# Optimization experiments

Measured on AMD Instinct MI355X. Metric: run time of the kernel, lower is better.

The kernel has to match this reference:

```python
import jax, jax.numpy as jnp
import numpy as np

B, L, D, A = 4, 4096, 256, 64  # batch, seq_len, n_embd, att_size

def setup_inputs() -> dict:
    key = jax.random.key(0)
    kx, kq, kk, kv = jax.random.split(key, 4)
    x = jax.random.normal(kx, (B, L, D), dtype=jnp.float32)
    # torch nn.Linear(n_embd, att_size) weight is [att_size, n_embd]; we store transposed [D, A]
    s = 1.0 / np.sqrt(D)
    Wq = jax.random.normal(kq, (D, A), dtype=jnp.float32) * s
    Wk = jax.random.normal(kk, (D, A), dtype=jnp.float32) * s
    Wv = jax.random.normal(kv, (D, A), dtype=jnp.float32) * s
    return {"x": x, "Wq": Wq, "Wk": Wk, "Wv": Wv}

def reference(x, Wq, Wk, Wv):
    # q,k,v: [B,L,A]
    q = jnp.einsum('bld,da->bla', x, Wq)
    k = jnp.einsum('bld,da->bla', x, Wk)
    v = jnp.einsum('bld,da->bla', x, Wv)
    # NOTE: original module does NOT scale by 1/sqrt(att_size)
    scores = jnp.einsum('bqa,bka->bqk', q, k)  # [B,L,L]
    Lq = x.shape[1]
    causal = jnp.tril(jnp.ones((Lq, Lq), dtype=bool))
    scores = jnp.where(causal, scores, -jnp.inf)
    weights = jax.nn.softmax(scores, axis=-1)
    # dropout is identity in eval mode
    out = jnp.einsum('bqk,bka->bqa', weights, v)  # [B,L,A]
    return out
```

## Files before the change

kernel.cpp:

```cpp
#include <hip/hip_runtime.h>
#include <math.h>

#define B_ 4
#define L_ 4096
#define D_ 256
#define A_ 64
#define M_ (B_*L_)

typedef _Float16 half4 __attribute__((ext_vector_type(4)));
typedef _Float16 half8 __attribute__((ext_vector_type(8)));
typedef __attribute__((ext_vector_type(4))) float floatx4;

__device__ __forceinline__ unsigned short f2h_(float f) {
    _Float16 h = (_Float16)f;
    return __builtin_bit_cast(unsigned short, h);
}

__global__ __launch_bounds__(256) void wconv_kernel(
    const float* __restrict__ Wq, const float* __restrict__ Wk,
    const float* __restrict__ Wv, unsigned short* __restrict__ wt)
{
    const int w = blockIdx.x, t = threadIdx.x;
    const float* W = (w == 0) ? Wq : (w == 1) ? Wk : Wv;
    unsigned short* o = wt + w * A_ * D_;
    const float scale = (w == 0) ? 1.44269504f : 1.0f;
    __shared__ float T[A_ * 260];
    #pragma unroll
    for (int p = 0; p < 16; ++p) {
        int idx = p * 256 + t;
        int d = idx >> 4, a4 = (idx & 15) * 4;
        float4 v = *(const float4*)(W + d * A_ + a4);
        T[(a4 + 0) * 260 + d] = v.x * scale;
        T[(a4 + 1) * 260 + d] = v.y * scale;
        T[(a4 + 2) * 260 + d] = v.z * scale;
        T[(a4 + 3) * 260 + d] = v.w * scale;
    }
    __syncthreads();
    const int a = t >> 2, d0 = (t & 3) * 64;
    #pragma unroll
    for (int i = 0; i < 16; ++i) {
        float4 v = *(const float4*)(&T[a * 260 + d0 + 4 * i]);
        ushort4 s;
        s.x = f2h_(v.x); s.y = f2h_(v.y); s.z = f2h_(v.z); s.w = f2h_(v.w);
        *(ushort4*)(o + a * D_ + d0 + 4 * i) = s;
    }
}

__global__ __launch_bounds__(384) void proj_kernel(
    const float* __restrict__ x,
    const unsigned short* __restrict__ wt,
    unsigned short* __restrict__ qo,
    unsigned short* __restrict__ ko,
    unsigned short* __restrict__ vto)
{
    __shared__ __align__(16) unsigned short Xh[32 * 264];
    __shared__ __align__(16) unsigned short Cst[6 * 1536];
    const int t = threadIdx.x, m0 = blockIdx.x * 32;

    #pragma unroll
    for (int p = 0; p < 6; ++p) {
        int idx = p * 384 + t;
        if (idx < 2048) {
            int row = idx >> 6, col = (idx & 63) * 4;
            float4 v = *(const float4*)(x + (size_t)(m0 + row) * D_ + col);
            ushort4 s;
            s.x = f2h_(v.x); s.y = f2h_(v.y); s.z = f2h_(v.z); s.w = f2h_(v.w);
            *(ushort4*)(Xh + row * 264 + col) = s;
        }
    }
    __syncthreads();

    const int wid = t >> 6, lane = t & 63, c = lane & 15, g = lane >> 4;
    const int w = wid >> 1, mt = wid & 1;

    half8 xa[8];
    #pragma unroll
    for (int s = 0; s < 8; ++s)
        xa[s] = *(const half8*)(Xh + (16 * mt + c) * 264 + 32 * s + 8 * g);

    const unsigned short* wsrc = wt + w * A_ * D_;
    unsigned short* Cw = Cst + wid * 1536;
    #pragma unroll
    for (int nt = 0; nt < 4; ++nt) {
        floatx4 acc = {0.f, 0.f, 0.f, 0.f};
        #pragma unroll
        for (int s = 0; s < 8; ++s) {
            half8 wb = *(const half8*)(wsrc + (16 * nt + c) * D_ + 32 * s + 8 * g);
            acc = __builtin_amdgcn_mfma_f32_16x16x32_f16(xa[s], wb, acc, 0, 0, 0);
        }
        if (w < 2) {
            #pragma unroll
            for (int r = 0; r < 4; ++r)
                Cw[(4 * g + r) * 72 + 16 * nt + c] = f2h_(acc[r]);
        } else {
            #pragma unroll
            for (int r = 0; r < 4; ++r)
                Cw[(16 * nt + c) * 24 + 4 * g + r] = f2h_(acc[r]);
        }
    }

    if (w < 2) {
        unsigned short* o = (w == 0) ? qo : ko;
        const int row16 = lane >> 2, seg = lane & 3;
        uint4 d0 = *(const uint4*)(Cw + row16 * 72 + seg * 16);
        uint4 d1 = *(const uint4*)(Cw + row16 * 72 + seg * 16 + 8);
        unsigned short* p = o + (size_t)(m0 + 16 * mt + row16) * A_ + seg * 16;
        *(uint4*)(p) = d0;
        *(uint4*)(p + 8) = d1;
    }
    __syncthreads();
    if (t < 256) {
        const int a = t >> 2, quarter = t & 3;
        const int o = quarter * 8, mtv = o >> 4, idx = o & 15;
        uint4 d = *(const uint4*)(Cst + (4 + mtv) * 1536 + a * 24 + idx);
        const int bb = m0 >> 12, l0 = m0 & (L_ - 1);
        *(uint4*)(vto + ((size_t)(bb * A_ + a)) * L_ + l0 + o) = d;
    }
}

__global__ __launch_bounds__(512) void attn_kernel(
    const unsigned short* __restrict__ qb,
    const unsigned short* __restrict__ kb,
    const unsigned short* __restrict__ vt,
    float* __restrict__ out,
    float* __restrict__ po1,
    float2* __restrict__ ml0,
    float2* __restrict__ ml1)
{
    __shared__ __align__(16) unsigned short smem[4 * 4608];
    unsigned short* Ks = smem;
    unsigned short* Vs = smem + 2 * 4608;

    const int t    = threadIdx.x;
    const int lane = t & 63;
    const int wid  = t >> 6;
    const int qsub = wid >> 1;
    const int ph   = wid & 1;
    const int c    = lane & 15;
    const int g    = lane >> 4;

    const int bx   = blockIdx.x;
    const int slot = bx & 255, rr = bx >> 8;
    const int qt0  = slot >> 2;
    const int h    = slot & 1;
    const int b    = ((slot >> 1) & 1) + 2 * rr;
    const int qt   = rr ? (63 - qt0) : qt0;

    const int q0    = qt * 64;
    const int qrow0 = q0 + 16 * qsub;
    const int qme   = qrow0 + c;

    const size_t base  = (size_t)b * L_ * A_;
    const size_t vbase = (size_t)b * A_ * L_;

    half8 qf[2];
    {
        const unsigned short* qp = qb + base + (size_t)(qrow0 + c) * A_ + g * 8;
        qf[0] = *(const half8*)(qp);
        qf[1] = *(const half8*)(qp + 32);
    }

    floatx4 O4[4];
    #pragma unroll
    for (int at = 0; at < 4; ++at) O4[at] = (floatx4){0.f, 0.f, 0.f, 0.f};
    float m_ = -INFINITY, l_ = 0.f;

    const int T   = qt + 1;
    const int Th  = (T + 1) >> 1;
    const int t0  = h ? Th : 0;
    const int t1  = h ? T : Th;
    const int nIt = (t1 - t0 + 1) >> 1;
    const int Tm1 = T - 1;

    for (int it = 0; it < nIt; ++it) {
        __syncthreads();
        #pragma unroll
        for (int tile = 0; tile < 2; ++tile) {
            const int kts = t0 + 2 * it + tile;
            if (kts < t1) {
                const int k0s = kts << 6;
                const int row = t >> 3, c8 = t & 7;
                uint4 dK = *(const uint4*)(kb + base + (size_t)k0s * 64 + t * 8);
                *(uint4*)(Ks + tile * 4608 + row * 72 + c8 * 8) = dK;
                uint4 dV = *(const uint4*)(vt + vbase + (size_t)row * L_ + k0s + c8 * 8);
                *(uint4*)(Vs + tile * 4608 + row * 72 + c8 * 8) = dV;
            }
        }
        __syncthreads();

        const int kt = t0 + 2 * it + ph;
        if (kt >= t1) continue;
        const int k0 = kt << 6;
        const unsigned short* Kw = Ks + ph * 4608;
        const unsigned short* Vw = Vs + ph * 4608;

        floatx4 S4[4];
        #pragma unroll
        for (int nt = 0; nt < 4; ++nt) S4[nt] = (floatx4){0.f, 0.f, 0.f, 0.f};
        #pragma unroll
        for (int s = 0; s < 2; ++s)
            #pragma unroll
            for (int nt = 0; nt < 4; ++nt) {
                half8 kf = *(const half8*)(Kw + (16 * nt + c) * 72 + 32 * s + 8 * g);
                S4[nt] = __builtin_amdgcn_mfma_f32_16x16x32_f16(kf, qf[s], S4[nt], 0, 0, 0);
            }

        if (kt == Tm1) {
            #pragma unroll
            for (int nt = 0; nt < 4; ++nt)
                #pragma unroll
                for (int r = 0; r < 4; ++r)
                    if (k0 + 16 * nt + 4 * g + r > qme) S4[nt][r] = -INFINITY;
        }

        float tm = fmaxf(fmaxf(fmaxf(S4[0][0], S4[0][1]), fmaxf(S4[0][2], S4[0][3])),
                         fmaxf(fmaxf(S4[1][0], S4[1][1]), fmaxf(S4[1][2], S4[1][3])));
        tm = fmaxf(tm, fmaxf(fmaxf(fmaxf(S4[2][0], S4[2][1]), fmaxf(S4[2][2], S4[2][3])),
                             fmaxf(fmaxf(S4[3][0], S4[3][1]), fmaxf(S4[3][2], S4[3][3]))));
        tm = fmaxf(tm, __shfl_xor(tm, 16));
        tm = fmaxf(tm, __shfl_xor(tm, 32));
        const float mn  = fmaxf(m_, tm);
        const float mnc = fmaxf(mn, -3.0e38f);
        const float al  = exp2f(fminf(m_ - mnc, 0.f));
        float rs = 0.f;
        half4 pf[4];
        #pragma unroll
        for (int nt = 0; nt < 4; ++nt) {
            #pragma unroll
            for (int r = 0; r < 4; ++r) {
                float p = exp2f(S4[nt][r] - mnc);
                S4[nt][r] = p;
                rs += p;
            }
            pf[nt][0] = (_Float16)S4[nt][0];
            pf[nt][1] = (_Float16)S4[nt][1];
            pf[nt][2] = (_Float16)S4[nt][2];
            pf[nt][3] = (_Float16)S4[nt][3];
        }
        rs += __shfl_xor(rs, 16);
        rs += __shfl_xor(rs, 32);
        l_ = l_ * al + rs;
        m_ = mn;

        #pragma unroll
        for (int at = 0; at < 4; ++at) {
            O4[at] *= al;
            #pragma unroll
            for (int nt = 0; nt < 4; ++nt) {
                half4 va = *(const half4*)(Vw + (16 * at + c) * 72 + 16 * nt + 4 * g);
                O4[at] = __builtin_amdgcn_mfma_f32_16x16x16f16(va, pf[nt], O4[at], 0, 0, 0);
            }
        }
    }

    __syncthreads();
    float*  Of  = (float*)smem;
    float2* mlb = (float2*)(smem + 16384);
    #pragma unroll
    for (int at = 0; at < 4; ++at) {
        float4 v; v.x = O4[at][0]; v.y = O4[at][1]; v.z = O4[at][2]; v.w = O4[at][3];
        ((float4*)Of)[wid * 256 + at * 64 + lane] = v;
    }
    if (g == 0) { float2 ml; ml.x = m_; ml.y = l_; mlb[wid * 16 + c] = ml; }
    __syncthreads();

    {
        const int q64 = t >> 3, seg = t & 7;
        const int qs = q64 >> 4, cc = q64 & 15;
        const float2 A0 = mlb[(2 * qs) * 16 + cc];
        const float2 A1 = mlb[(2 * qs + 1) * 16 + cc];
        const float mf = fmaxf(A0.x, A1.x);
        const float mc = fmaxf(mf, -3.0e38f);
        const float w0 = exp2f(A0.x - mc);
        const float w1 = exp2f(A1.x - mc);
        const float ls = w0 * A0.y + w1 * A1.y;
        float res[8];
        #pragma unroll
        for (int u = 0; u < 8; ++u) {
            const int a = seg * 8 + u;
            const int at = a >> 4, gg = (a >> 2) & 3, r = a & 3;
            const int i0 = ((2 * qs) * 256 + at * 64 + gg * 16 + cc) * 4 + r;
            const int i1 = ((2 * qs + 1) * 256 + at * 64 + gg * 16 + cc) * 4 + r;
            res[u] = w0 * Of[i0] + w1 * Of[i1];
        }
        float* PO = h ? po1 : out;
        float* p = PO + (base + (size_t)(q0 + q64) * A_) + seg * 8;
        *(float4*)(p)     = make_float4(res[0], res[1], res[2], res[3]);
        *(float4*)(p + 4) = make_float4(res[4], res[5], res[6], res[7]);
        if (seg == 0) {
            float2 ml; ml.x = mf; ml.y = ls;
            (h ? ml1 : ml0)[b * L_ + q0 + q64] = ml;
        }
    }
}

__global__ __launch_bounds__(256) void merge_kernel(
    float* __restrict__ out, const float* __restrict__ po1,
    const float2* __restrict__ ml0, const float2* __restrict__ ml1)
{
    const int tg = blockIdx.x * 256 + threadIdx.x;
    const int q = tg >> 4;
    const float2 a0 = ml0[q], a1 = ml1[q];
    const float mf = fmaxf(a0.x, a1.x);
    const float mc = fmaxf(mf, -3.0e38f);
    const float w0 = exp2f(a0.x - mc);
    const float w1 = exp2f(a1.x - mc);
    const float inv = 1.f / (w0 * a0.y + w1 * a1.y);
    float4 o0 = ((const float4*)out)[tg];
    float4 o1 = ((const float4*)po1)[tg];
    float4 r;
    r.x = (o0.x * w0 + o1.x * w1) * inv;
    r.y = (o0.y * w0 + o1.y * w1) * inv;
    r.z = (o0.z * w0 + o1.z * w1) * inv;
    r.w = (o0.w * w0 + o1.w * w1) * inv;
    ((float4*)out)[tg] = r;
}

extern "C" void kernel_launch(void* const* d_in, const int* in_sizes, int n_in,
                              void* d_out, int out_size, void* d_ws, size_t ws_size,
                              hipStream_t stream) {
    const float* x  = (const float*)d_in[0];
    const float* Wq = (const float*)d_in[1];
    const float* Wk = (const float*)d_in[2];
    const float* Wv = (const float*)d_in[3];

    char* ws = (char*)d_ws;
    unsigned short* qb = (unsigned short*)(ws);
    unsigned short* kb = (unsigned short*)(ws + (2u << 20));
    unsigned short* vt = (unsigned short*)(ws + (4u << 20));
    unsigned short* wt = (unsigned short*)(ws + (6u << 20));
    float*  po1 = (float*) (ws + (6u << 20) + 98304);
    float2* ml0 = (float2*)(ws + (6u << 20) + 98304 + (4u << 20));
    float2* ml1 = (float2*)(ws + (6u << 20) + 98304 + (4u << 20) + 131072);
    float* out = (float*)d_out;

    hipLaunchKernelGGL(wconv_kernel, dim3(3), dim3(256), 0, stream, Wq, Wk, Wv, wt);
    hipLaunchKernelGGL(proj_kernel, dim3(M_ / 32), dim3(384), 0, stream, x, wt, qb, kb, vt);
    hipLaunchKernelGGL(attn_kernel, dim3(512), dim3(512), 0, stream,
                       qb, kb, vt, out, po1, ml0, ml1);
    hipLaunchKernelGGL(merge_kernel, dim3(1024), dim3(256), 0, stream, out, po1, ml0, ml1);
}
```

Measured before the change: 124.8 us.

## Split attention KV range four ways instead of two and merge four partials

Each query tile's causal KV range is now split into four chunks, handled by 1024 blocks instead of 512, with the block-to-(batch, tile, split) mapping reworked. The merge kernel combines four partial outputs and their max/sum stats. The aim is more parallelism and better load balance across CUs for the triangular workload. The cost is extra partial-output traffic, more workspace, and a heavier merge. Tiles with few KV blocks get empty or tiny splits.

```diff
diff --git a/kernel.cpp b/kernel.cpp
--- a/kernel.cpp
+++ b/kernel.cpp
@@ -124,8 +124,12 @@
     const unsigned short* __restrict__ vt,
     float* __restrict__ out,
     float* __restrict__ po1,
+    float* __restrict__ po2,
+    float* __restrict__ po3,
     float2* __restrict__ ml0,
-    float2* __restrict__ ml1)
+    float2* __restrict__ ml1,
+    float2* __restrict__ ml2,
+    float2* __restrict__ ml3)
 {
     __shared__ __align__(16) unsigned short smem[4 * 4608];
     unsigned short* Ks = smem;
@@ -142,9 +146,9 @@
     const int bx   = blockIdx.x;
     const int slot = bx & 255, rr = bx >> 8;
     const int qt0  = slot >> 2;
-    const int h    = slot & 1;
-    const int b    = ((slot >> 1) & 1) + 2 * rr;
-    const int qt   = rr ? (63 - qt0) : qt0;
+    const int b    = slot & 3;
+    const int h    = rr;
+    const int qt   = (rr < 2) ? qt0 : (63 - qt0);
 
     const int q0    = qt * 64;
     const int qrow0 = q0 + 16 * qsub;
@@ -166,9 +170,8 @@
     float m_ = -INFINITY, l_ = 0.f;
 
     const int T   = qt + 1;
-    const int Th  = (T + 1) >> 1;
-    const int t0  = h ? Th : 0;
-    const int t1  = h ? T : Th;
+    const int t0  = (h * T) >> 2;
+    const int t1  = ((h + 1) * T) >> 2;
     const int nIt = (t1 - t0 + 1) >> 1;
     const int Tm1 = T - 1;
 
@@ -283,36 +286,43 @@
             const int i1 = ((2 * qs + 1) * 256 + at * 64 + gg * 16 + cc) * 4 + r;
             res[u] = w0 * Of[i0] + w1 * Of[i1];
         }
-        float* PO = h ? po1 : out;
+        float* PO = (h == 0) ? out : (h == 1) ? po1 : (h == 2) ? po2 : po3;
         float* p = PO + (base + (size_t)(q0 + q64) * A_) + seg * 8;
         *(float4*)(p)     = make_float4(res[0], res[1], res[2], res[3]);
         *(float4*)(p + 4) = make_float4(res[4], res[5], res[6], res[7]);
         if (seg == 0) {
             float2 ml; ml.x = mf; ml.y = ls;
-            (h ? ml1 : ml0)[b * L_ + q0 + q64] = ml;
+            float2* MLp = (h == 0) ? ml0 : (h == 1) ? ml1 : (h == 2) ? ml2 : ml3;
+            MLp[b * L_ + q0 + q64] = ml;
         }
     }
 }
 
 __global__ __launch_bounds__(256) void merge_kernel(
     float* __restrict__ out, const float* __restrict__ po1,
-    const float2* __restrict__ ml0, const float2* __restrict__ ml1)
+    const float* __restrict__ po2, const float* __restrict__ po3,
+    const float2* __restrict__ ml0, const float2* __restrict__ ml1,
+    const float2* __restrict__ ml2, const float2* __restrict__ ml3)
 {
     const int tg = blockIdx.x * 256 + threadIdx.x;
     const int q = tg >> 4;
-    const float2 a0 = ml0[q], a1 = ml1[q];
-    const float mf = fmaxf(a0.x, a1.x);
+    const float2 a0 = ml0[q], a1 = ml1[q], a2 = ml2[q], a3 = ml3[q];
+    const float mf = fmaxf(fmaxf(a0.x, a1.x), fmaxf(a2.x, a3.x));
     const float mc = fmaxf(mf, -3.0e38f);
     const float w0 = exp2f(a0.x - mc);
     const float w1 = exp2f(a1.x - mc);
-    const float inv = 1.f / (w0 * a0.y + w1 * a1.y);
+    const float w2 = exp2f(a2.x - mc);
+    const float w3 = exp2f(a3.x - mc);
+    const float inv = 1.f / (w0 * a0.y + w1 * a1.y + w2 * a2.y + w3 * a3.y);
     float4 o0 = ((const float4*)out)[tg];
     float4 o1 = ((const float4*)po1)[tg];
+    float4 o2 = ((const float4*)po2)[tg];
+    float4 o3 = ((const float4*)po3)[tg];
     float4 r;
-    r.x = (o0.x * w0 + o1.x * w1) * inv;
-    r.y = (o0.y * w0 + o1.y * w1) * inv;
-    r.z = (o0.z * w0 + o1.z * w1) * inv;
-    r.w = (o0.w * w0 + o1.w * w1) * inv;
+    r.x = (o0.x * w0 + o1.x * w1 + o2.x * w2 + o3.x * w3) * inv;
+    r.y = (o0.y * w0 + o1.y * w1 + o2.y * w2 + o3.y * w3) * inv;
+    r.z = (o0.z * w0 + o1.z * w1 + o2.z * w2 + o3.z * w3) * inv;
+    r.w = (o0.w * w0 + o1.w * w1 + o2.w * w2 + o3.w * w3) * inv;
     ((float4*)out)[tg] = r;
 }
 
@@ -329,14 +339,21 @@
     unsigned short* kb = (unsigned short*)(ws + (2u << 20));
     unsigned short* vt = (unsigned short*)(ws + (4u << 20));
     unsigned short* wt = (unsigned short*)(ws + (6u << 20));
-    float*  po1 = (float*) (ws + (6u << 20) + 98304);
-    float2* ml0 = (float2*)(ws + (6u << 20) + 98304 + (4u << 20));
-    float2* ml1 = (float2*)(ws + (6u << 20) + 98304 + (4u << 20) + 131072);
+    char* p0 = ws + (6u << 20) + (128u << 10);
+    float* po1 = (float*)(p0);
+    float* po2 = (float*)(p0 + (4u << 20));
+    float* po3 = (float*)(p0 + (8u << 20));
+    char* p1 = p0 + (12u << 20);
+    float2* ml0 = (float2*)(p1);
+    float2* ml1 = (float2*)(p1 + (128u << 10));
+    float2* ml2 = (float2*)(p1 + (256u << 10));
+    float2* ml3 = (float2*)(p1 + (384u << 10));
     float* out = (float*)d_out;
 
     hipLaunchKernelGGL(wconv_kernel, dim3(3), dim3(256), 0, stream, Wq, Wk, Wv, wt);
     hipLaunchKernelGGL(proj_kernel, dim3(M_ / 32), dim3(384), 0, stream, x, wt, qb, kb, vt);
-    hipLaunchKernelGGL(attn_kernel, dim3(512), dim3(512), 0, stream,
-                       qb, kb, vt, out, po1, ml0, ml1);
-    hipLaunchKernelGGL(merge_kernel, dim3(1024), dim3(256), 0, stream, out, po1, ml0, ml1);
-}
+    hipLaunchKernelGGL(attn_kernel, dim3(1024), dim3(512), 0, stream,
+                       qb, kb, vt, out, po1, po2, po3, ml0, ml1, ml2, ml3);
+    hipLaunchKernelGGL(merge_kernel, dim3(1024), dim3(256), 0, stream,
+                       out, po1, po2, po3, ml0, ml1, ml2, ml3);
+}
```

Result: no change. 123.6 us (-1.0%).

## Split causal key range into variable chunks per query tile for load balance

Applied to the files above, without the earlier changes.

Replaces the fixed two-way key split per query tile with a variable split. Each query tile qt gets floor(qt/8)+1 key chunks, giving 1152 roughly equal-work blocks, ordered from heaviest to lightest. Partial outputs and softmax stats go to per-chunk workspace buffers, and the merge kernel combines up to 8 partials per row. This should balance work across CUs and raise parallelism, at the cost of more partial-output traffic, a larger workspace (32MB) and a heavier merge.

```diff
diff --git a/kernel.cpp b/kernel.cpp
--- a/kernel.cpp
+++ b/kernel.cpp
@@ -122,10 +122,8 @@
     const unsigned short* __restrict__ qb,
     const unsigned short* __restrict__ kb,
     const unsigned short* __restrict__ vt,
-    float* __restrict__ out,
-    float* __restrict__ po1,
-    float2* __restrict__ ml0,
-    float2* __restrict__ ml1)
+    float* __restrict__ poB,
+    float2* __restrict__ mlB)
 {
     __shared__ __align__(16) unsigned short smem[4 * 4608];
     unsigned short* Ks = smem;
@@ -139,12 +137,21 @@
     const int c    = lane & 15;
     const int g    = lane >> 4;
 
-    const int bx   = blockIdx.x;
-    const int slot = bx & 255, rr = bx >> 8;
-    const int qt0  = slot >> 2;
-    const int h    = slot & 1;
-    const int b    = ((slot >> 1) & 1) + 2 * rr;
-    const int qt   = rr ? (63 - qt0) : qt0;
+    const int bx = blockIdx.x;
+    const int x  = bx & 7, u = bx >> 3;
+    const int b  = x >> 1;
+    const int gch = 287 - (2 * u + (x & 1));
+    int m = 0;
+    while (4 * (m + 1) * (m + 2) <= gch) ++m;
+    const int rem = gch - 4 * m * (m + 1);
+    const int nch = m + 1;
+    const int qt  = 8 * m + rem / nch;
+    const int j   = rem % nch;
+    const int T   = qt + 1;
+    const int t0  = (j * T) / nch;
+    const int t1  = ((j + 1) * T) / nch;
+    const int nIt = (t1 - t0 + 1) >> 1;
+    const int Tm1 = T - 1;
 
     const int q0    = qt * 64;
     const int qrow0 = q0 + 16 * qsub;
@@ -164,13 +171,6 @@
     #pragma unroll
     for (int at = 0; at < 4; ++at) O4[at] = (floatx4){0.f, 0.f, 0.f, 0.f};
     float m_ = -INFINITY, l_ = 0.f;
-
-    const int T   = qt + 1;
-    const int Th  = (T + 1) >> 1;
-    const int t0  = h ? Th : 0;
-    const int t1  = h ? T : Th;
-    const int nIt = (t1 - t0 + 1) >> 1;
-    const int Tm1 = T - 1;
 
     for (int it = 0; it < nIt; ++it) {
         __syncthreads();
@@ -276,43 +276,50 @@
         const float ls = w0 * A0.y + w1 * A1.y;
         float res[8];
         #pragma unroll
-        for (int u = 0; u < 8; ++u) {
-            const int a = seg * 8 + u;
+        for (int u2 = 0; u2 < 8; ++u2) {
+            const int a = seg * 8 + u2;
             const int at = a >> 4, gg = (a >> 2) & 3, r = a & 3;
             const int i0 = ((2 * qs) * 256 + at * 64 + gg * 16 + cc) * 4 + r;
             const int i1 = ((2 * qs + 1) * 256 + at * 64 + gg * 16 + cc) * 4 + r;
-            res[u] = w0 * Of[i0] + w1 * Of[i1];
-        }
-        float* PO = h ? po1 : out;
-        float* p = PO + (base + (size_t)(q0 + q64) * A_) + seg * 8;
+            res[u2] = w0 * Of[i0] + w1 * Of[i1];
+        }
+        float* p = poB + (size_t)j * M_ * A_ + base + (size_t)(q0 + q64) * A_ + seg * 8;
         *(float4*)(p)     = make_float4(res[0], res[1], res[2], res[3]);
         *(float4*)(p + 4) = make_float4(res[4], res[5], res[6], res[7]);
         if (seg == 0) {
             float2 ml; ml.x = mf; ml.y = ls;
-            (h ? ml1 : ml0)[b * L_ + q0 + q64] = ml;
+            mlB[(size_t)j * M_ + b * L_ + q0 + q64] = ml;
         }
     }
 }
 
 __global__ __launch_bounds__(256) void merge_kernel(
-    float* __restrict__ out, const float* __restrict__ po1,
-    const float2* __restrict__ ml0, const float2* __restrict__ ml1)
+    float* __restrict__ out, const float* __restrict__ poB,
+    const float2* __restrict__ mlB)
 {
     const int tg = blockIdx.x * 256 + threadIdx.x;
     const int q = tg >> 4;
-    const float2 a0 = ml0[q], a1 = ml1[q];
-    const float mf = fmaxf(a0.x, a1.x);
+    const int qt = (q & (L_ - 1)) >> 6;
+    const int nch = (qt + 8) >> 3;
+    float2 a[8];
+    float mf = -INFINITY;
+    for (int jj = 0; jj < nch; ++jj) {
+        a[jj] = mlB[(size_t)jj * M_ + q];
+        mf = fmaxf(mf, a[jj].x);
+    }
     const float mc = fmaxf(mf, -3.0e38f);
-    const float w0 = exp2f(a0.x - mc);
-    const float w1 = exp2f(a1.x - mc);
-    const float inv = 1.f / (w0 * a0.y + w1 * a1.y);
-    float4 o0 = ((const float4*)out)[tg];
-    float4 o1 = ((const float4*)po1)[tg];
+    float den = 0.f;
+    float4 acc = make_float4(0.f, 0.f, 0.f, 0.f);
+    for (int jj = 0; jj < nch; ++jj) {
+        const float wj = exp2f(a[jj].x - mc);
+        den += wj * a[jj].y;
+        const float4 o = ((const float4*)(poB + (size_t)jj * M_ * A_))[tg];
+        acc.x += o.x * wj; acc.y += o.y * wj;
+        acc.z += o.z * wj; acc.w += o.w * wj;
+    }
+    const float inv = 1.f / den;
     float4 r;
-    r.x = (o0.x * w0 + o1.x * w1) * inv;
-    r.y = (o0.y * w0 + o1.y * w1) * inv;
-    r.z = (o0.z * w0 + o1.z * w1) * inv;
-    r.w = (o0.w * w0 + o1.w * w1) * inv;
+    r.x = acc.x * inv; r.y = acc.y * inv; r.z = acc.z * inv; r.w = acc.w * inv;
     ((float4*)out)[tg] = r;
 }
 
@@ -329,14 +336,15 @@
     unsigned short* kb = (unsigned short*)(ws + (2u << 20));
     unsigned short* vt = (unsigned short*)(ws + (4u << 20));
     unsigned short* wt = (unsigned short*)(ws + (6u << 20));
-    float*  po1 = (float*) (ws + (6u << 20) + 98304);
-    float2* ml0 = (float2*)(ws + (6u << 20) + 98304 + (4u << 20));
-    float2* ml1 = (float2*)(ws + (6u << 20) + 98304 + (4u << 20) + 131072);
+    char* p0 = ws + (6u << 20) + (128u << 10);
+    float*  poB = (float*)(p0);
+    float2* mlB = (float2*)(p0 + (32u << 20));
     float* out = (float*)d_out;
 
     hipLaunchKernelGGL(wconv_kernel, dim3(3), dim3(256), 0, stream, Wq, Wk, Wv, wt);
     hipLaunchKernelGGL(proj_kernel, dim3(M_ / 32), dim3(384), 0, stream, x, wt, qb, kb, vt);
-    hipLaunchKernelGGL(attn_kernel, dim3(512), dim3(512), 0, stream,
-                       qb, kb, vt, out, po1, ml0, ml1);
-    hipLaunchKernelGGL(merge_kernel, dim3(1024), dim3(256), 0, stream, out, po1, ml0, ml1);
-}
+    hipLaunchKernelGGL(attn_kernel, dim3(1152), dim3(512), 0, stream,
+                       qb, kb, vt, poB, mlB);
+    hipLaunchKernelGGL(merge_kernel, dim3(1024), dim3(256), 0, stream,
+                       out, poB, mlB);
+}
```

Result: slower. 147.6 us (+18.3%).
